# Kernel optimization log

Measured on AMD Instinct MI355X. Metric: run time of the kernel, lower is better.

Reference implementation:

```python
import jax, jax.numpy as jnp
import numpy as np

B, N, C = 16, 4096, 64
M, K, R = 1024, 32, 0.2
EPS = 1e-5  # BatchNorm eps (eval mode: running_mean=0, running_var=1)


def setup_inputs() -> dict:
    key = jax.random.key(0)
    ks = jax.random.split(key, 8)
    s = 0.05
    return {
        "points": jax.random.normal(ks[0], (B, 3, N), dtype=jnp.float32),
        "features": jax.random.normal(ks[1], (B, C, N), dtype=jnp.float32),
        "w1": jax.random.normal(ks[2], (64, 3 + C), dtype=jnp.float32) * s,
        "b1": jnp.zeros((64,), jnp.float32),
        "g1": jnp.ones((64,), jnp.float32),
        "be1": jnp.zeros((64,), jnp.float32),
        "w2": jax.random.normal(ks[3], (64, 64), dtype=jnp.float32) * s,
        "b2": jnp.zeros((64,), jnp.float32),
        "g2": jnp.ones((64,), jnp.float32),
        "be2": jnp.zeros((64,), jnp.float32),
        "w3": jax.random.normal(ks[4], (128, 64), dtype=jnp.float32) * s,
        "b3": jnp.zeros((128,), jnp.float32),
        "g3": jnp.ones((128,), jnp.float32),
        "be3": jnp.zeros((128,), jnp.float32),
    }


def farthest_point_sampling(pts, m):
    """pts: [B,N,3] -> indices [B,m] (iterative FPS, first point = index 0)."""
    b, n, _ = pts.shape

    def step(carry, _):
        dist, last = carry  # dist [b,n], last [b]
        lastp = jnp.take_along_axis(pts, last[:, None, None], axis=1)  # [b,1,3]
        d = jnp.sum((pts - lastp) ** 2, axis=-1)  # [b,n]
        dist = jnp.minimum(dist, d)
        nxt = jnp.argmax(dist, axis=1).astype(jnp.int32)
        return (dist, nxt), last

    init = (jnp.full((b, n), 1e10, pts.dtype), jnp.zeros((b,), jnp.int32))
    _, idx = jax.lax.scan(step, init, None, length=m)
    return idx.T  # [b,m]


def ball_query(pts, centroids, k, radius):
    """pts [B,N,3], centroids [B,M,3] -> neighbor indices [B,M,K].
    Takes the first k points (by index) within radius; pads with the first hit,
    matching the PointNet++ CUDA ball_query semantics."""
    n = pts.shape[1]
    p2 = jnp.sum(pts ** 2, -1)  # [B,N]
    c2 = jnp.sum(centroids ** 2, -1)  # [B,M]
    d2 = c2[:, :, None] + p2[:, None, :] - 2.0 * jnp.einsum("bmd,bnd->bmn", centroids, pts)
    ar = jnp.arange(n, dtype=jnp.int32)
    key = jnp.where(d2 <= radius * radius, ar[None, None, :], n)  # [B,M,N]
    idx = jnp.sort(key, axis=-1)[..., :k]  # first k in-radius indices (or n)
    first = idx[..., :1]  # centroid itself is always a hit (d2=0)
    idx = jnp.where(idx < n, idx, first)
    return jnp.clip(idx, 0, n - 1)


def _mlp_block(x, w, bias, g, be):
    # 1x1 Conv2d + BatchNorm (eval: mean=0, var=1) + ReLU, x: [B,M,K,Cin]
    y = jnp.einsum("oc,bmkc->bmko", w, x) + bias
    y = y * (g / jnp.sqrt(1.0 + EPS)) + be
    return jax.nn.relu(y)


def reference(points, features, w1, b1, g1, be1, w2, b2, g2, be2, w3, b3, g3, be3):
    pts = jnp.transpose(points, (0, 2, 1))  # [B,N,3]
    feats = jnp.transpose(features, (0, 2, 1))  # [B,N,C]
    b = pts.shape[0]

    cidx = farthest_point_sampling(pts, M)  # [B,M]
    bidx = jnp.arange(b)[:, None]
    cent = pts[bidx, cidx]  # [B,M,3]

    nidx = ball_query(pts, cent, K, R)  # [B,M,K]
    bidx2 = jnp.arange(b)[:, None, None]
    gpts = pts[bidx2, nidx]  # [B,M,K,3]
    gfeat = feats[bidx2, nidx]  # [B,M,K,C]
    local = gpts - cent[:, :, None, :]  # local coords
    x = jnp.concatenate([local, gfeat], axis=-1)  # [B,M,K,3+C]

    x = _mlp_block(x, w1, b1, g1, be1)
    x = _mlp_block(x, w2, b2, g2, be2)
    x = _mlp_block(x, w3, b3, g3, be3)

    out = jnp.max(x, axis=2)  # max over K samples -> [B,M,Cout]
    centroids = jnp.transpose(cent, (0, 2, 1))  # [B,3,M]
    out = jnp.transpose(out, (0, 2, 1))  # [B,Cout,M]
    return centroids, out
```

## Files before the change

kernel.cpp:

```cpp
#include <hip/hip_runtime.h>
#include <math.h>

#define NPTS 4096
#define MC   1024
#define KNB  32

typedef __attribute__((ext_vector_type(8))) short bf16x8;
typedef __attribute__((ext_vector_type(4))) float f32x4;

__device__ __forceinline__ unsigned short f2bf(float f) {
  unsigned int u = __float_as_uint(f);
  u = u + 0x7fffu + ((u >> 16) & 1u);
  return (unsigned short)(u >> 16);
}

template <int CTRL>
__device__ __forceinline__ float dpp_max(float v) {
  int o = __builtin_amdgcn_update_dpp(__float_as_int(v), __float_as_int(v), CTRL, 0xF, 0xF, false);
  return fmaxf(v, __int_as_float(o));
}

struct FpsShared {
  float sx[NPTS], sy[NPTS], sz[NPTS];
  unsigned long long skey[2][4];
  float slog[3][MC];
};
struct TransShared {
  float tile[64][65];
};

__global__ __launch_bounds__(256, 1) void fused_pre(
    const float* __restrict__ points, const float* __restrict__ feats,
    const float* __restrict__ w1, const float* __restrict__ w2,
    const float* __restrict__ w3,
    unsigned short* __restrict__ featsT, unsigned short* __restrict__ wpack,
    float* __restrict__ out_cent) {
  __shared__ union { FpsShared f; TransShared tr; } S;
  const int blk = blockIdx.x;
  const int t = threadIdx.x;

  if (blk < 16) {
    const int b = blk;
    const int w = t >> 6;
    const float* pb = points + (size_t)b * 3 * NPTS;

    float fx[16], fy[16], fz[16], dist[16];
#pragma unroll
    for (int k = 0; k < 4; ++k) {
      float4 X = ((const float4*)pb)[k * 256 + t];
      float4 Y = ((const float4*)(pb + NPTS))[k * 256 + t];
      float4 Z = ((const float4*)(pb + 2 * NPTS))[k * 256 + t];
      ((float4*)S.f.sx)[k * 256 + t] = X;
      ((float4*)S.f.sy)[k * 256 + t] = Y;
      ((float4*)S.f.sz)[k * 256 + t] = Z;
      fx[k * 4 + 0] = X.x; fx[k * 4 + 1] = X.y; fx[k * 4 + 2] = X.z; fx[k * 4 + 3] = X.w;
      fy[k * 4 + 0] = Y.x; fy[k * 4 + 1] = Y.y; fy[k * 4 + 2] = Y.z; fy[k * 4 + 3] = Y.w;
      fz[k * 4 + 0] = Z.x; fz[k * 4 + 1] = Z.y; fz[k * 4 + 2] = Z.z; fz[k * 4 + 3] = Z.w;
    }
#pragma unroll
    for (int j = 0; j < 16; ++j) dist[j] = 1e10f;
    __syncthreads();

    float lx = S.f.sx[0], ly = S.f.sy[0], lz = S.f.sz[0];

    for (int i = 0; i < MC; ++i) {
      if (t == 0) { S.f.slog[0][i] = lx; S.f.slog[1][i] = ly; S.f.slog[2][i] = lz; }
      if (i == MC - 1) break;

      float m = -1.0f;
#pragma unroll
      for (int j = 0; j < 16; ++j) {
        float dx = __fsub_rn(fx[j], lx);
        float dy = __fsub_rn(fy[j], ly);
        float dz = __fsub_rn(fz[j], lz);
        float d  = __fadd_rn(__fadd_rn(__fmul_rn(dx, dx), __fmul_rn(dy, dy)), __fmul_rn(dz, dz));
        float dm = fminf(dist[j], d);
        dist[j] = dm;
        m = fmaxf(m, dm);
      }

      m = dpp_max<0x111>(m);
      m = dpp_max<0x112>(m);
      m = dpp_max<0x114>(m);
      m = dpp_max<0x118>(m);
      m = dpp_max<0x142>(m);
      m = dpp_max<0x143>(m);
      const float wv = __int_as_float(__builtin_amdgcn_readlane(__float_as_int(m), 63));

      unsigned long long mk[4][4];
#pragma unroll
      for (int k = 0; k < 4; ++k) {
        mk[k][0] = __ballot(dist[k * 4 + 0] == wv);
        mk[k][1] = __ballot(dist[k * 4 + 1] == wv);
        mk[k][2] = __ballot(dist[k * 4 + 2] == wv);
        mk[k][3] = __ballot(dist[k * 4 + 3] == wv);
      }
      unsigned long long s0 = 0, s1 = 0, s2 = 0, s3 = 0, anyk = 0;
      int sk = -1;
#pragma unroll
      for (int k = 0; k < 4; ++k) {
        unsigned long long a = mk[k][0] | mk[k][1] | mk[k][2] | mk[k][3];
        if (sk < 0 && a != 0ull) {
          sk = k; anyk = a;
          s0 = mk[k][0]; s1 = mk[k][1]; s2 = mk[k][2]; s3 = mk[k][3];
        }
      }
      const int l = __builtin_ctzll(anyk);
      const unsigned long long bit = 1ull << l;
      const int c = (s0 & bit) ? 0 : (s1 & bit) ? 1 : (s2 & bit) ? 2 : 3;
      const int selIdx = sk * 1024 + 256 * w + 4 * l + c;

      const int nb = i & 1;
      if ((t & 63) == 0)
        S.f.skey[nb][w] = ((unsigned long long)__float_as_uint(wv) << 32) | (unsigned int)~selIdx;
      __syncthreads();

      unsigned long long k0 = S.f.skey[nb][0], k1 = S.f.skey[nb][1];
      unsigned long long k2 = S.f.skey[nb][2], k3 = S.f.skey[nb][3];
      unsigned long long ka = (k0 > k1) ? k0 : k1;
      unsigned long long kb = (k2 > k3) ? k2 : k3;
      unsigned long long km = (ka > kb) ? ka : kb;
      const int sel = (int)(~(unsigned int)km);
      lx = S.f.sx[sel]; ly = S.f.sy[sel]; lz = S.f.sz[sel];
    }
    __syncthreads();
    float* oc = out_cent + (size_t)b * 3 * MC;
#pragma unroll
    for (int k = 0; k < 12; ++k) {
      int idx = t + k * 256;
      oc[idx] = ((const float*)S.f.slog)[idx];
    }
  } else if (blk < 16 + 1024) {
    const int rel = blk - 16;
    const int b = rel >> 6;
    const int n0 = (rel & 63) * 64;
    const float* src = feats + (size_t)b * 64 * NPTS;
    {
      const int n = t & 63, cbase = t >> 6;
#pragma unroll
      for (int j = 0; j < 16; ++j) {
        int cc = cbase + j * 4;
        S.tr.tile[cc][n] = src[(size_t)cc * NPTS + n0 + n];
      }
    }
    __syncthreads();
    {
      const int cc = t & 63, nbase = t >> 6;
      unsigned short* dst = featsT + ((size_t)b * NPTS + n0) * 64;
#pragma unroll
      for (int j = 0; j < 16; ++j) {
        int n = nbase + j * 4;
        dst[(size_t)n * 64 + cc] = f2bf(S.tr.tile[cc][n]);
      }
    }
  } else {
    const int f = (blk - (16 + 1024)) * 4 + (t >> 6);
    const int lane = t & 63;
    if (f < 36) {
      int layer, kt, nt;
      if (f < 12)      { layer = 0; kt = f >> 2;        nt = f & 3; }
      else if (f < 20) { layer = 1; kt = (f - 12) >> 2; nt = (f - 12) & 3; }
      else             { layer = 2; kt = (f - 20) >> 3; nt = (f - 20) & 7; }
      const int o = nt * 16 + (lane & 15);
      unsigned short* dst = wpack + ((size_t)f * 64 + lane) * 8;
#pragma unroll
      for (int j = 0; j < 8; ++j) {
        int k = kt * 32 + (lane >> 4) * 8 + j;
        float x = 0.0f;
        if (layer == 0)      { if (k < 67) { int cin = (k < 64) ? (k + 3) : (k - 64); x = w1[o * 67 + cin]; } }
        else if (layer == 1) { x = w2[o * 64 + k]; }
        else                 { x = w3[o * 64 + k]; }
        dst[j] = f2bf(x);
      }
    }
  }
}

struct PtsS { float sx[NPTS], sy[NPTS], sz[NPTS]; };
struct MlpS { unsigned short Hs[4][2][32 * 72]; float obuf[128 * 20]; };

__global__ __launch_bounds__(256, 1) void mlp_bq_kernel(
    const float* __restrict__ points,
    const float* __restrict__ cent,
    const unsigned short* __restrict__ featsT,
    const unsigned short* __restrict__ wpack,
    const float* __restrict__ b1, const float* __restrict__ g1, const float* __restrict__ be1,
    const float* __restrict__ b2, const float* __restrict__ g2, const float* __restrict__ be2,
    const float* __restrict__ b3, const float* __restrict__ g3, const float* __restrict__ be3,
    float* __restrict__ out) {
  __shared__ __align__(16) union { PtsS p; MlpS d; } U;
  __shared__ int lists[4][KNB];
  const int t = threadIdx.x;
  const int w = t >> 6, lane = t & 63;
  const int r = lane & 15, q = lane >> 4;
  const float inv_s = 1.0f / sqrtf(1.0f + 1e-5f);

  const int bm0 = blockIdx.x * 16;
  const int b   = bm0 >> 10;
  const int m0  = bm0 & 1023;
  const float* cbp = cent + (size_t)b * 3 * MC;

  {
    const float* pb = points + (size_t)b * 3 * NPTS;
#pragma unroll
    for (int j = 0; j < 4; ++j) {
      int i4 = t + j * 256;
      ((float4*)U.p.sx)[i4] = ((const float4*)pb)[i4];
      ((float4*)U.p.sy)[i4] = ((const float4*)(pb + NPTS))[i4];
      ((float4*)U.p.sz)[i4] = ((const float4*)(pb + 2 * NPTS))[i4];
    }
  }
  __syncthreads();

  int n0r[4], n1r[4];
  bf16x8 aL[4][2];
  const float R2 = (float)(0.2 * 0.2);
#pragma unroll
  for (int it = 0; it < 4; ++it) {
    const int m = m0 + it * 4 + w;
    const float cx = cbp[m], cy = cbp[MC + m], cz = cbp[2 * MC + m];
    const float c2 = __fadd_rn(__fadd_rn(__fmul_rn(cx, cx), __fmul_rn(cy, cy)), __fmul_rn(cz, cz));
    int cnt = 0;
    for (int ch = 0; ch < 64; ++ch) {
      const int n = ch * 64 + lane;
      float x = U.p.sx[n], y = U.p.sy[n], z = U.p.sz[n];
      float p2  = __fadd_rn(__fadd_rn(__fmul_rn(x, x),  __fmul_rn(y, y)),  __fmul_rn(z, z));
      float dot = __fadd_rn(__fadd_rn(__fmul_rn(cx, x), __fmul_rn(cy, y)), __fmul_rn(cz, z));
      float d2  = __fsub_rn(__fadd_rn(c2, p2), __fmul_rn(2.0f, dot));
      bool hit = (d2 <= R2);
      unsigned long long msk = __ballot(hit);
      if (hit) {
        int pos = cnt + __popcll(msk & ((1ull << lane) - 1ull));
        if (pos < KNB) lists[w][pos] = n;
      }
      cnt += __popcll(msk);
      if (cnt >= KNB) break;
    }
    {
      int first = lists[w][0];
      if (lane < KNB) {
        int v = (lane < cnt) ? lists[w][lane] : first;
        lists[w][lane] = v;
      }
    }
    const int n0 = lists[w][r];
    const int n1 = lists[w][16 + r];
    n0r[it] = n0; n1r[it] = n1;
#pragma unroll
    for (int mt = 0; mt < 2; ++mt) {
      bf16x8 a = {0, 0, 0, 0, 0, 0, 0, 0};
      if (q == 0) {
        int n = mt ? n1 : n0;
        a[0] = (short)f2bf(U.p.sx[n] - cx);
        a[1] = (short)f2bf(U.p.sy[n] - cy);
        a[2] = (short)f2bf(U.p.sz[n] - cz);
      }
      aL[it][mt] = a;
    }
  }
  __syncthreads();

  float pb1[4], ps1[4], pe1[4], pb2[4], ps2[4], pe2[4], pb3[8], ps3[8], pe3[8];
#pragma unroll
  for (int nt = 0; nt < 4; ++nt) {
    int o = nt * 16 + r;
    pb1[nt] = b1[o]; ps1[nt] = g1[o] * inv_s; pe1[nt] = be1[o];
    pb2[nt] = b2[o]; ps2[nt] = g2[o] * inv_s; pe2[nt] = be2[o];
  }
#pragma unroll
  for (int nt = 0; nt < 8; ++nt) {
    int o = nt * 16 + r;
    pb3[nt] = b3[o]; ps3[nt] = g3[o] * inv_s; pe3[nt] = be3[o];
  }

  for (int it = 0; it < 4; ++it) {
    const int ml = it * 4 + w;
    const int n0 = n0r[it], n1 = n1r[it];

    bf16x8 aF[2][2];
#pragma unroll
    for (int mt = 0; mt < 2; ++mt) {
      int n = mt ? n1 : n0;
      const unsigned short* rowp = featsT + ((size_t)b * NPTS + n) * 64 + q * 8;
      aF[mt][0] = *(const bf16x8*)(rowp);
      aF[mt][1] = *(const bf16x8*)(rowp + 32);
    }
    f32x4 acc1[2][4];
#pragma unroll
    for (int mt = 0; mt < 2; ++mt)
#pragma unroll
      for (int nt = 0; nt < 4; ++nt) acc1[mt][nt] = (f32x4){0.f, 0.f, 0.f, 0.f};
#pragma unroll
    for (int kt = 0; kt < 3; ++kt) {
#pragma unroll
      for (int nt = 0; nt < 4; ++nt) {
        bf16x8 wf = *(const bf16x8*)(wpack + ((size_t)(kt * 4 + nt) * 64 + lane) * 8);
#pragma unroll
        for (int mt = 0; mt < 2; ++mt) {
          bf16x8 a = (kt < 2) ? aF[mt][kt] : aL[it][mt];
          acc1[mt][nt] = __builtin_amdgcn_mfma_f32_16x16x32_bf16(a, wf, acc1[mt][nt], 0, 0, 0);
        }
      }
    }
#pragma unroll
    for (int mt = 0; mt < 2; ++mt)
#pragma unroll
      for (int nt = 0; nt < 4; ++nt)
#pragma unroll
        for (int rr = 0; rr < 4; ++rr) {
          float y = (acc1[mt][nt][rr] + pb1[nt]) * ps1[nt] + pe1[nt];
          y = fmaxf(y, 0.0f);
          U.d.Hs[w][0][(mt * 16 + q * 4 + rr) * 72 + nt * 16 + r] = f2bf(y);
        }
    __threadfence_block();

    f32x4 acc2[2][4];
#pragma unroll
    for (int mt = 0; mt < 2; ++mt)
#pragma unroll
      for (int nt = 0; nt < 4; ++nt) acc2[mt][nt] = (f32x4){0.f, 0.f, 0.f, 0.f};
#pragma unroll
    for (int kt = 0; kt < 2; ++kt) {
      bf16x8 a0 = *(const bf16x8*)&U.d.Hs[w][0][(0 * 16 + r) * 72 + kt * 32 + q * 8];
      bf16x8 a1 = *(const bf16x8*)&U.d.Hs[w][0][(1 * 16 + r) * 72 + kt * 32 + q * 8];
#pragma unroll
      for (int nt = 0; nt < 4; ++nt) {
        bf16x8 wf = *(const bf16x8*)(wpack + ((size_t)(12 + kt * 4 + nt) * 64 + lane) * 8);
        acc2[0][nt] = __builtin_amdgcn_mfma_f32_16x16x32_bf16(a0, wf, acc2[0][nt], 0, 0, 0);
        acc2[1][nt] = __builtin_amdgcn_mfma_f32_16x16x32_bf16(a1, wf, acc2[1][nt], 0, 0, 0);
      }
    }
#pragma unroll
    for (int mt = 0; mt < 2; ++mt)
#pragma unroll
      for (int nt = 0; nt < 4; ++nt)
#pragma unroll
        for (int rr = 0; rr < 4; ++rr) {
          float y = (acc2[mt][nt][rr] + pb2[nt]) * ps2[nt] + pe2[nt];
          y = fmaxf(y, 0.0f);
          U.d.Hs[w][1][(mt * 16 + q * 4 + rr) * 72 + nt * 16 + r] = f2bf(y);
        }
    __threadfence_block();

    f32x4 acc3[2][8];
#pragma unroll
    for (int mt = 0; mt < 2; ++mt)
#pragma unroll
      for (int nt = 0; nt < 8; ++nt) acc3[mt][nt] = (f32x4){0.f, 0.f, 0.f, 0.f};
#pragma unroll
    for (int kt = 0; kt < 2; ++kt) {
      bf16x8 a0 = *(const bf16x8*)&U.d.Hs[w][1][(0 * 16 + r) * 72 + kt * 32 + q * 8];
      bf16x8 a1 = *(const bf16x8*)&U.d.Hs[w][1][(1 * 16 + r) * 72 + kt * 32 + q * 8];
#pragma unroll
      for (int nt = 0; nt < 8; ++nt) {
        bf16x8 wf = *(const bf16x8*)(wpack + ((size_t)(20 + kt * 8 + nt) * 64 + lane) * 8);
        acc3[0][nt] = __builtin_amdgcn_mfma_f32_16x16x32_bf16(a0, wf, acc3[0][nt], 0, 0, 0);
        acc3[1][nt] = __builtin_amdgcn_mfma_f32_16x16x32_bf16(a1, wf, acc3[1][nt], 0, 0, 0);
      }
    }
#pragma unroll
    for (int nt = 0; nt < 8; ++nt) {
      float pm = 0.0f;
#pragma unroll
      for (int mt = 0; mt < 2; ++mt)
#pragma unroll
        for (int rr = 0; rr < 4; ++rr) {
          float y = (acc3[mt][nt][rr] + pb3[nt]) * ps3[nt] + pe3[nt];
          y = fmaxf(y, 0.0f);
          pm = fmaxf(pm, y);
        }
      pm = fmaxf(pm, __shfl_xor(pm, 16));
      pm = fmaxf(pm, __shfl_xor(pm, 32));
      if (q == 0) U.d.obuf[(nt * 16 + r) * 20 + ml] = pm;
    }
    __threadfence_block();
  }
  __syncthreads();
  {
    const int ch = t >> 1, mh = (t & 1) * 8;
    float4 u0 = *(const float4*)&U.d.obuf[ch * 20 + mh];
    float4 u1 = *(const float4*)&U.d.obuf[ch * 20 + mh + 4];
    float* outp = out + ((size_t)b * 128 + ch) * 1024 + m0 + mh;
    *(float4*)(outp)     = u0;
    *(float4*)(outp + 4) = u1;
  }
}

extern "C" void kernel_launch(void* const* d_in, const int* in_sizes, int n_in,
                              void* d_out, int out_size, void* d_ws, size_t ws_size,
                              hipStream_t stream) {
  (void)in_sizes; (void)n_in; (void)out_size; (void)ws_size;
  const float* points   = (const float*)d_in[0];
  const float* features = (const float*)d_in[1];
  const float* w1  = (const float*)d_in[2];
  const float* b1  = (const float*)d_in[3];
  const float* g1  = (const float*)d_in[4];
  const float* be1 = (const float*)d_in[5];
  const float* w2  = (const float*)d_in[6];
  const float* b2  = (const float*)d_in[7];
  const float* g2  = (const float*)d_in[8];
  const float* be2 = (const float*)d_in[9];
  const float* w3  = (const float*)d_in[10];
  const float* b3  = (const float*)d_in[11];
  const float* g3  = (const float*)d_in[12];
  const float* be3 = (const float*)d_in[13];

  float* outc = (float*)d_out;
  float* outf = outc + 16 * 3 * 1024;

  char* ws = (char*)d_ws;
  unsigned short* featsT  = (unsigned short*)(ws);
  unsigned short* wpack   = (unsigned short*)(ws + 0x800000);

  fused_pre<<<16 + 1024 + 9, 256, 0, stream>>>(points, features, w1, w2, w3,
                                               featsT, wpack, outc);
  mlp_bq_kernel<<<1024, 256, 0, stream>>>(points, outc, featsT, wpack,
                                          b1, g1, be1, b2, g2, be2,
                                          b3, g3, be3, outf);
}
```

Baseline: 1.060 ms.

## Fuse FPS and MLP into one persistent kernel with progress-flag streaming

Merges the preprocessing and ball-query/MLP kernels into a single launch. The FPS blocks publish centroids every 16 iterations through an agent-scope release counter, and the consumer blocks spin-wait only until their own centroids are ready. The transpose and weight-packing work is folded into the first 128 consumer blocks, which signal completion through a second counter. This overlaps the serial FPS with ball query and MLP instead of running them back to back. It depends on all 1040 blocks being co-resident or scheduled in a safe order, so spin-waiting can deadlock or stall if they are not.

Result: slower. 1.122 ms (+5.8%).

```diff
diff --git a/kernel.cpp b/kernel.cpp
--- a/kernel.cpp
+++ b/kernel.cpp
@@ -4,6 +4,7 @@
 #define NPTS 4096
 #define MC   1024
 #define KNB  32
+#define AGT  __HIP_MEMORY_SCOPE_AGENT
 
 typedef __attribute__((ext_vector_type(8))) short bf16x8;
 typedef __attribute__((ext_vector_type(4))) float f32x4;
@@ -25,24 +26,30 @@
   unsigned long long skey[2][4];
   float slog[3][MC];
 };
-struct TransShared {
-  float tile[64][65];
-};
-
-__global__ __launch_bounds__(256, 1) void fused_pre(
+struct TransShared { float tile[64][65]; };
+struct PtsS { float sx[NPTS], sy[NPTS], sz[NPTS]; };
+struct MlpS { unsigned short Hs[4][2][32 * 72]; float obuf[128 * 20]; };
+
+__global__ __launch_bounds__(256, 1) void mega(
     const float* __restrict__ points, const float* __restrict__ feats,
     const float* __restrict__ w1, const float* __restrict__ w2,
     const float* __restrict__ w3,
+    const float* __restrict__ b1, const float* __restrict__ g1, const float* __restrict__ be1,
+    const float* __restrict__ b2, const float* __restrict__ g2, const float* __restrict__ be2,
+    const float* __restrict__ b3, const float* __restrict__ g3, const float* __restrict__ be3,
     unsigned short* __restrict__ featsT, unsigned short* __restrict__ wpack,
-    float* __restrict__ out_cent) {
-  __shared__ union { FpsShared f; TransShared tr; } S;
+    float* __restrict__ out_cent, float* __restrict__ out_feat,
+    unsigned int* __restrict__ prog, unsigned int* __restrict__ preCnt) {
+  __shared__ union { FpsShared f; TransShared tr; PtsS p; MlpS d; } S;
+  __shared__ int lists[4][KNB];
   const int blk = blockIdx.x;
   const int t = threadIdx.x;
+  const int w = t >> 6, lane = t & 63;
 
   if (blk < 16) {
     const int b = blk;
-    const int w = t >> 6;
     const float* pb = points + (size_t)b * 3 * NPTS;
+    float* oc = out_cent + (size_t)b * 3 * MC;
 
     float fx[16], fy[16], fz[16], dist[16];
 #pragma unroll
@@ -65,6 +72,14 @@
 
     for (int i = 0; i < MC; ++i) {
       if (t == 0) { S.f.slog[0][i] = lx; S.f.slog[1][i] = ly; S.f.slog[2][i] = lz; }
+      if ((i & 15) == 15) {
+        if (t < 48) {
+          const int coord = t >> 4, mm = (i & ~15) + (t & 15);
+          oc[coord * MC + mm] = S.f.slog[coord][mm];
+        }
+        if (t == 0)
+          __hip_atomic_store(&prog[b], (unsigned)(i + 1), __ATOMIC_RELEASE, AGT);
+      }
       if (i == MC - 1) break;
 
       float m = -1.0f;
@@ -123,92 +138,86 @@
       const int sel = (int)(~(unsigned int)km);
       lx = S.f.sx[sel]; ly = S.f.sy[sel]; lz = S.f.sz[sel];
     }
+    return;
+  }
+
+  const int rel = blk - 16;
+
+  if (rel < 128) {
+    for (int j = 0; j < 8; ++j) {
+      const int T = rel * 8 + j;
+      const int tb = T >> 6;
+      const int n0t = (T & 63) * 64;
+      const float* src = feats + (size_t)tb * 64 * NPTS;
+      {
+        const int n = t & 63, cbase = t >> 6;
+#pragma unroll
+        for (int jj = 0; jj < 16; ++jj) {
+          int cc = cbase + jj * 4;
+          S.tr.tile[cc][n] = src[(size_t)cc * NPTS + n0t + n];
+        }
+      }
+      __syncthreads();
+      {
+        const int cc = t & 63, nbase = t >> 6;
+        unsigned short* dst = featsT + ((size_t)tb * NPTS + n0t) * 64;
+#pragma unroll
+        for (int jj = 0; jj < 16; ++jj) {
+          int n = nbase + jj * 4;
+          dst[(size_t)n * 64 + cc] = f2bf(S.tr.tile[cc][n]);
+        }
+      }
+      __syncthreads();
+    }
+    if (rel < 9) {
+      const int f = rel * 4 + w;
+      if (f < 36) {
+        int layer, kt, nt;
+        if (f < 12)      { layer = 0; kt = f >> 2;        nt = f & 3; }
+        else if (f < 20) { layer = 1; kt = (f - 12) >> 2; nt = (f - 12) & 3; }
+        else             { layer = 2; kt = (f - 20) >> 3; nt = (f - 20) & 7; }
+        const int o = nt * 16 + (lane & 15);
+        unsigned short* dst = wpack + ((size_t)f * 64 + lane) * 8;
+#pragma unroll
+        for (int j = 0; j < 8; ++j) {
+          int k = kt * 32 + (lane >> 4) * 8 + j;
+          float x = 0.0f;
+          if (layer == 0)      { if (k < 67) { int cin = (k < 64) ? (k + 3) : (k - 64); x = w1[o * 67 + cin]; } }
+          else if (layer == 1) { x = w2[o * 64 + k]; }
+          else                 { x = w3[o * 64 + k]; }
+          dst[j] = f2bf(x);
+        }
+      }
+    }
     __syncthreads();
-    float* oc = out_cent + (size_t)b * 3 * MC;
-#pragma unroll
-    for (int k = 0; k < 12; ++k) {
-      int idx = t + k * 256;
-      oc[idx] = ((const float*)S.f.slog)[idx];
-    }
-  } else if (blk < 16 + 1024) {
-    const int rel = blk - 16;
-    const int b = rel >> 6;
-    const int n0 = (rel & 63) * 64;
-    const float* src = feats + (size_t)b * 64 * NPTS;
-    {
-      const int n = t & 63, cbase = t >> 6;
-#pragma unroll
-      for (int j = 0; j < 16; ++j) {
-        int cc = cbase + j * 4;
-        S.tr.tile[cc][n] = src[(size_t)cc * NPTS + n0 + n];
-      }
-    }
-    __syncthreads();
-    {
-      const int cc = t & 63, nbase = t >> 6;
-      unsigned short* dst = featsT + ((size_t)b * NPTS + n0) * 64;
-#pragma unroll
-      for (int j = 0; j < 16; ++j) {
-        int n = nbase + j * 4;
-        dst[(size_t)n * 64 + cc] = f2bf(S.tr.tile[cc][n]);
-      }
-    }
-  } else {
-    const int f = (blk - (16 + 1024)) * 4 + (t >> 6);
-    const int lane = t & 63;
-    if (f < 36) {
-      int layer, kt, nt;
-      if (f < 12)      { layer = 0; kt = f >> 2;        nt = f & 3; }
-      else if (f < 20) { layer = 1; kt = (f - 12) >> 2; nt = (f - 12) & 3; }
-      else             { layer = 2; kt = (f - 20) >> 3; nt = (f - 20) & 7; }
-      const int o = nt * 16 + (lane & 15);
-      unsigned short* dst = wpack + ((size_t)f * 64 + lane) * 8;
-#pragma unroll
-      for (int j = 0; j < 8; ++j) {
-        int k = kt * 32 + (lane >> 4) * 8 + j;
-        float x = 0.0f;
-        if (layer == 0)      { if (k < 67) { int cin = (k < 64) ? (k + 3) : (k - 64); x = w1[o * 67 + cin]; } }
-        else if (layer == 1) { x = w2[o * 64 + k]; }
-        else                 { x = w3[o * 64 + k]; }
-        dst[j] = f2bf(x);
-      }
-    }
-  }
-}
-
-struct PtsS { float sx[NPTS], sy[NPTS], sz[NPTS]; };
-struct MlpS { unsigned short Hs[4][2][32 * 72]; float obuf[128 * 20]; };
-
-__global__ __launch_bounds__(256, 1) void mlp_bq_kernel(
-    const float* __restrict__ points,
-    const float* __restrict__ cent,
-    const unsigned short* __restrict__ featsT,
-    const unsigned short* __restrict__ wpack,
-    const float* __restrict__ b1, const float* __restrict__ g1, const float* __restrict__ be1,
-    const float* __restrict__ b2, const float* __restrict__ g2, const float* __restrict__ be2,
-    const float* __restrict__ b3, const float* __restrict__ g3, const float* __restrict__ be3,
-    float* __restrict__ out) {
-  __shared__ __align__(16) union { PtsS p; MlpS d; } U;
-  __shared__ int lists[4][KNB];
-  const int t = threadIdx.x;
-  const int w = t >> 6, lane = t & 63;
-  const int r = lane & 15, q = lane >> 4;
-  const float inv_s = 1.0f / sqrtf(1.0f + 1e-5f);
-
-  const int bm0 = blockIdx.x * 16;
+    if (t == 0) {
+      unsigned add = 8u + ((rel < 9) ? 4u : 0u);
+      __hip_atomic_fetch_add(preCnt, add, __ATOMIC_RELEASE, AGT);
+    }
+  }
+
+  const int bm0 = rel * 16;
   const int b   = bm0 >> 10;
   const int m0  = bm0 & 1023;
-  const float* cbp = cent + (size_t)b * 3 * MC;
+  const float* cbp = out_cent + (size_t)b * 3 * MC;
+  const int r = lane & 15, q = lane >> 4;
 
   {
     const float* pb = points + (size_t)b * 3 * NPTS;
+    __syncthreads();
 #pragma unroll
     for (int j = 0; j < 4; ++j) {
       int i4 = t + j * 256;
-      ((float4*)U.p.sx)[i4] = ((const float4*)pb)[i4];
-      ((float4*)U.p.sy)[i4] = ((const float4*)(pb + NPTS))[i4];
-      ((float4*)U.p.sz)[i4] = ((const float4*)(pb + 2 * NPTS))[i4];
-    }
+      ((float4*)S.p.sx)[i4] = ((const float4*)pb)[i4];
+      ((float4*)S.p.sy)[i4] = ((const float4*)(pb + NPTS))[i4];
+      ((float4*)S.p.sz)[i4] = ((const float4*)(pb + 2 * NPTS))[i4];
+    }
+  }
+  __syncthreads();
+
+  if (t == 0) {
+    while (__hip_atomic_load(&prog[b], __ATOMIC_ACQUIRE, AGT) < (unsigned)(m0 + 16))
+      __builtin_amdgcn_s_sleep(16);
   }
   __syncthreads();
 
@@ -223,7 +232,7 @@
     int cnt = 0;
     for (int ch = 0; ch < 64; ++ch) {
       const int n = ch * 64 + lane;
-      float x = U.p.sx[n], y = U.p.sy[n], z = U.p.sz[n];
+      float x = S.p.sx[n], y = S.p.sy[n], z = S.p.sz[n];
       float p2  = __fadd_rn(__fadd_rn(__fmul_rn(x, x),  __fmul_rn(y, y)),  __fmul_rn(z, z));
       float dot = __fadd_rn(__fadd_rn(__fmul_rn(cx, x), __fmul_rn(cy, y)), __fmul_rn(cz, z));
       float d2  = __fsub_rn(__fadd_rn(c2, p2), __fmul_rn(2.0f, dot));
@@ -251,15 +260,22 @@
       bf16x8 a = {0, 0, 0, 0, 0, 0, 0, 0};
       if (q == 0) {
         int n = mt ? n1 : n0;
-        a[0] = (short)f2bf(U.p.sx[n] - cx);
-        a[1] = (short)f2bf(U.p.sy[n] - cy);
-        a[2] = (short)f2bf(U.p.sz[n] - cz);
+        a[0] = (short)f2bf(S.p.sx[n] - cx);
+        a[1] = (short)f2bf(S.p.sy[n] - cy);
+        a[2] = (short)f2bf(S.p.sz[n] - cz);
       }
       aL[it][mt] = a;
     }
   }
   __syncthreads();
 
+  if (t == 0) {
+    while (__hip_atomic_load(preCnt, __ATOMIC_ACQUIRE, AGT) < 1060u)
+      __builtin_amdgcn_s_sleep(16);
+  }
+  __syncthreads();
+
+  const float inv_s = 1.0f / sqrtf(1.0f + 1e-5f);
   float pb1[4], ps1[4], pe1[4], pb2[4], ps2[4], pe2[4], pb3[8], ps3[8], pe3[8];
 #pragma unroll
   for (int nt = 0; nt < 4; ++nt) {
@@ -310,7 +326,7 @@
         for (int rr = 0; rr < 4; ++rr) {
           float y = (acc1[mt][nt][rr] + pb1[nt]) * ps1[nt] + pe1[nt];
           y = fmaxf(y, 0.0f);
-          U.d.Hs[w][0][(mt * 16 + q * 4 + rr) * 72 + nt * 16 + r] = f2bf(y);
+          S.d.Hs[w][0][(mt * 16 + q * 4 + rr) * 72 + nt * 16 + r] = f2bf(y);
         }
     __threadfence_block();
 
@@ -321,8 +337,8 @@
       for (int nt = 0; nt < 4; ++nt) acc2[mt][nt] = (f32x4){0.f, 0.f, 0.f, 0.f};
 #pragma unroll
     for (int kt = 0; kt < 2; ++kt) {
-      bf16x8 a0 = *(const bf16x8*)&U.d.Hs[w][0][(0 * 16 + r) * 72 + kt * 32 + q * 8];
-      bf16x8 a1 = *(const bf16x8*)&U.d.Hs[w][0][(1 * 16 + r) * 72 + kt * 32 + q * 8];
+      bf16x8 a0 = *(const bf16x8*)&S.d.Hs[w][0][(0 * 16 + r) * 72 + kt * 32 + q * 8];
+      bf16x8 a1 = *(const bf16x8*)&S.d.Hs[w][0][(1 * 16 + r) * 72 + kt * 32 + q * 8];
 #pragma unroll
       for (int nt = 0; nt < 4; ++nt) {
         bf16x8 wf = *(const bf16x8*)(wpack + ((size_t)(12 + kt * 4 + nt) * 64 + lane) * 8);
@@ -338,7 +354,7 @@
         for (int rr = 0; rr < 4; ++rr) {
           float y = (acc2[mt][nt][rr] + pb2[nt]) * ps2[nt] + pe2[nt];
           y = fmaxf(y, 0.0f);
-          U.d.Hs[w][1][(mt * 16 + q * 4 + rr) * 72 + nt * 16 + r] = f2bf(y);
+          S.d.Hs[w][1][(mt * 16 + q * 4 + rr) * 72 + nt * 16 + r] = f2bf(y);
         }
     __threadfence_block();
 
@@ -349,8 +365,8 @@
       for (int nt = 0; nt < 8; ++nt) acc3[mt][nt] = (f32x4){0.f, 0.f, 0.f, 0.f};
 #pragma unroll
     for (int kt = 0; kt < 2; ++kt) {
-      bf16x8 a0 = *(const bf16x8*)&U.d.Hs[w][1][(0 * 16 + r) * 72 + kt * 32 + q * 8];
-      bf16x8 a1 = *(const bf16x8*)&U.d.Hs[w][1][(1 * 16 + r) * 72 + kt * 32 + q * 8];
+      bf16x8 a0 = *(const bf16x8*)&S.d.Hs[w][1][(0 * 16 + r) * 72 + kt * 32 + q * 8];
+      bf16x8 a1 = *(const bf16x8*)&S.d.Hs[w][1][(1 * 16 + r) * 72 + kt * 32 + q * 8];
 #pragma unroll
       for (int nt = 0; nt < 8; ++nt) {
         bf16x8 wf = *(const bf16x8*)(wpack + ((size_t)(20 + kt * 8 + nt) * 64 + lane) * 8);
@@ -371,16 +387,16 @@
         }
       pm = fmaxf(pm, __shfl_xor(pm, 16));
       pm = fmaxf(pm, __shfl_xor(pm, 32));
-      if (q == 0) U.d.obuf[(nt * 16 + r) * 20 + ml] = pm;
+      if (q == 0) S.d.obuf[(nt * 16 + r) * 20 + ml] = pm;
     }
     __threadfence_block();
   }
   __syncthreads();
   {
     const int ch = t >> 1, mh = (t & 1) * 8;
-    float4 u0 = *(const float4*)&U.d.obuf[ch * 20 + mh];
-    float4 u1 = *(const float4*)&U.d.obuf[ch * 20 + mh + 4];
-    float* outp = out + ((size_t)b * 128 + ch) * 1024 + m0 + mh;
+    float4 u0 = *(const float4*)&S.d.obuf[ch * 20 + mh];
+    float4 u1 = *(const float4*)&S.d.obuf[ch * 20 + mh + 4];
+    float* outp = out_feat + ((size_t)b * 128 + ch) * 1024 + m0 + mh;
     *(float4*)(outp)     = u0;
     *(float4*)(outp + 4) = u1;
   }
@@ -409,12 +425,13 @@
   float* outf = outc + 16 * 3 * 1024;
 
   char* ws = (char*)d_ws;
-  unsigned short* featsT  = (unsigned short*)(ws);
-  unsigned short* wpack   = (unsigned short*)(ws + 0x800000);
-
-  fused_pre<<<16 + 1024 + 9, 256, 0, stream>>>(points, features, w1, w2, w3,
-                                               featsT, wpack, outc);
-  mlp_bq_kernel<<<1024, 256, 0, stream>>>(points, outc, featsT, wpack,
-                                          b1, g1, be1, b2, g2, be2,
-                                          b3, g3, be3, outf);
+  unsigned short* featsT = (unsigned short*)(ws);
+  unsigned short* wpack  = (unsigned short*)(ws + 0x800000);
+  unsigned int*   prog   = (unsigned int*)(ws + 0x810000);
+  unsigned int*   preCnt = (unsigned int*)(ws + 0x810040);
+
+  hipMemsetAsync(ws + 0x810000, 0, 0x80, stream);
+  mega<<<16 + 1024, 256, 0, stream>>>(points, features, w1, w2, w3,
+                                      b1, g1, be1, b2, g2, be2, b3, g3, be3,
+                                      featsT, wpack, outc, outf, prog, preCnt);
 }
```
